# Kernel optimization log

Measured on AMD Instinct MI355X. Metric: run time of the kernel, lower is better.

The kernel has to match this reference:

```python
import jax, jax.numpy as jnp
import numpy as np
from jax import lax

C = 64; H = 128; W = 256; HW = H * W
HIDDEN = 64
D_STATE = 64; HEADDIM = 64; EXPAND = 2; CHUNK = 256; CONV_K = 4
D_INNER = EXPAND * C            # 128
NHEADS = D_INNER // HEADDIM     # 2
CONV_DIM = D_INNER + 2 * D_STATE  # 256
D_IN_PROJ = 2 * D_INNER + 2 * D_STATE + NHEADS  # 386
RECORD_LEN = [5, 3, 4, 2]
EPS = 1e-5


def setup_inputs() -> dict:
    key = jax.random.key(0)
    ks = jax.random.split(key, 16)
    def nrm(k, shape, scale=0.02):
        return scale * jax.random.normal(k, shape, jnp.float32)
    return {
        "xx": jax.random.normal(ks[0], (sum(RECORD_LEN), C, H, W), jnp.float32),
        "record_len": jnp.array(RECORD_LEN, jnp.int32),
        "score_w1": nrm(ks[1], (HIDDEN, C)),
        "score_b1": jnp.zeros((HIDDEN,), jnp.float32),
        "score_w2": nrm(ks[2], (1, HIDDEN)),
        "score_b2": jnp.zeros((1,), jnp.float32),
        "q_w": nrm(ks[3], (C, C)), "q_b": jnp.zeros((C,), jnp.float32),
        "k_w": nrm(ks[4], (C, C)), "k_b": jnp.zeros((C,), jnp.float32),
        "v_w": nrm(ks[5], (C, C)), "v_b": jnp.zeros((C,), jnp.float32),
        "ln_w": jnp.ones((C,), jnp.float32), "ln_b": jnp.zeros((C,), jnp.float32),
        "in_proj_w": nrm(ks[6], (D_IN_PROJ, C)),
        "in_proj_b": jnp.zeros((D_IN_PROJ,), jnp.float32),
        "conv_w": nrm(ks[7], (CONV_DIM, 1, CONV_K), 0.1),
        "conv_b": jnp.zeros((CONV_DIM,), jnp.float32),
        "dt_bias": 0.1 * jax.random.normal(ks[8], (NHEADS,), jnp.float32),
        "A_log": jnp.log(jnp.arange(1, NHEADS + 1, dtype=jnp.float32)),
        "ssd_D": jnp.ones((NHEADS,), jnp.float32),
        "rms_w": jnp.ones((D_INNER,), jnp.float32),
        "out_proj_w": nrm(ks[9], (C, D_INNER)),
    }


def _segsum(x):
    # x: (..., T) -> (..., T, T) with sum_{j<k<=i} x[k] below diagonal, -inf above
    T = x.shape[-1]
    cs = jnp.cumsum(x, -1)
    ss = cs[..., :, None] - cs[..., None, :]
    return jnp.where(jnp.tril(jnp.ones((T, T), bool)), ss, -jnp.inf)


def _ssd(x, A, Bm, Cm):
    # Mamba2 chunked SSD. x:(b,l,h,p) pre-scaled by dt; A:(b,l,h)=dt*A_head; Bm,Cm:(b,l,n) (ngroups=1)
    b, l, h, p = x.shape
    c = l // CHUNK
    x = x.reshape(b, c, CHUNK, h, p)
    A = A.reshape(b, c, CHUNK, h).transpose(0, 3, 1, 2)            # (b,h,c,cl)
    Bm = Bm.reshape(b, c, CHUNK, -1)
    Cm = Cm.reshape(b, c, CHUNK, -1)
    A_cum = jnp.cumsum(A, -1)
    Lmat = jnp.exp(_segsum(A))                                     # (b,h,c,cl,cl)
    Y_diag = jnp.einsum('bcln,bcsn,bhcls,bcshp->bclhp', Cm, Bm, Lmat, x)
    decay_states = jnp.exp(A_cum[..., -1:] - A_cum)                # (b,h,c,cl)
    states = jnp.einsum('bcln,bhcl,bclhp->bchpn', Bm, decay_states, x)
    padded = jnp.pad(A_cum[..., -1], ((0, 0), (0, 0), (1, 0)))     # (b,h,c+1)
    decay_chunk = jnp.exp(_segsum(padded))                         # (b,h,c+1,c+1)
    states_cat = jnp.concatenate([jnp.zeros_like(states[:, :1]), states], 1)
    states_in = jnp.einsum('bhzc,bchpn->bzhpn', decay_chunk, states_cat)[:, :-1]
    Y_off = jnp.einsum('bcln,bchpn,bhcl->bclhp', Cm, states_in, jnp.exp(A_cum))
    return (Y_diag + Y_off).reshape(b, l, h, p)


def _forward(xx, record_len, score_w1, score_b1, score_w2, score_b2,
             q_w, q_b, k_w, k_b, v_w, v_b, ln_w, ln_b,
             in_proj_w, in_proj_b, conv_w, conv_b,
             dt_bias, A_log, ssd_D, rms_w, out_proj_w):
    rl = [int(v) for v in np.asarray(record_len)]
    # score_mlp: 1x1 convs == per-pixel channel MLP, applied to all CAVs at once
    s = jax.nn.relu(jnp.einsum('nchw,dc->ndhw', xx, score_w1) + score_b1[None, :, None, None])
    scores = (jnp.einsum('ndhw,od->nohw', s, score_w2) + score_b2[None, :, None, None])[:, 0]  # (N,H,W)
    fused = []
    start = 0
    for n in rl:  # ragged groups (variable n_cav per sample)
        grp_sc = scores[start:start + n]
        idx = jnp.argmax(grp_sc, axis=0)  # topk k=1; softmax over singleton -> weight 1
        fused.append(jnp.take_along_axis(xx[start:start + n], idx[None, None], axis=0)[0])
        start += n
    fused = jnp.stack(fused)  # (B,C,H,W)
    Bsz = fused.shape[0]
    seq = fused.reshape(Bsz, C, HW).transpose(0, 2, 1)  # (B,L,C)
    # ScaledDotProductAttention on (HW,1,C): each position attends only to itself
    q = seq @ q_w.T + q_b
    k = seq @ k_w.T + k_b
    v = seq @ v_w.T + v_b
    score = jnp.sum(q * k, -1, keepdims=True) / np.float32(np.sqrt(C))  # (B,L,1)
    attn = jax.nn.softmax(score[..., None], axis=-1)[..., 0]            # == 1
    ctx = attn * v
    # VMAMBA2 block: pre-LayerNorm -> Mamba2 SSD -> residual
    mu = jnp.mean(ctx, -1, keepdims=True)
    var = jnp.var(ctx, -1, keepdims=True)
    u = (ctx - mu) / jnp.sqrt(var + EPS) * ln_w + ln_b
    zxbcdt = u @ in_proj_w.T + in_proj_b
    z = zxbcdt[..., :D_INNER]
    xBC = zxbcdt[..., D_INNER:D_INNER + CONV_DIM]
    dt = zxbcdt[..., D_INNER + CONV_DIM:]
    xBC = lax.conv_general_dilated(xBC.transpose(0, 2, 1), conv_w, (1,), [(CONV_K - 1, 0)],
                                   dimension_numbers=('NCH', 'OIH', 'NCH'),
                                   feature_group_count=CONV_DIM)
    xBC = jax.nn.silu(xBC + conv_b[None, :, None]).transpose(0, 2, 1)  # (B,L,CONV_DIM)
    xh = xBC[..., :D_INNER].reshape(Bsz, HW, NHEADS, HEADDIM)
    Bm = xBC[..., D_INNER:D_INNER + D_STATE]
    Cm = xBC[..., D_INNER + D_STATE:]
    dt = jax.nn.softplus(dt + dt_bias)  # (B,L,h)
    A = -jnp.exp(A_log)                 # (h,)
    y = _ssd(xh * dt[..., None], dt * A, Bm, Cm)
    y = y + ssd_D[None, None, :, None] * xh
    y = y.reshape(Bsz, HW, D_INNER)
    yz = y * jax.nn.silu(z)             # gated RMSNorm
    y = yz * lax.rsqrt(jnp.mean(yz * yz, -1, keepdims=True) + EPS) * rms_w
    h = ctx + y @ out_proj_w.T
    return h.transpose(0, 2, 1).reshape(Bsz, C, H, W)


def reference(xx, record_len, score_w1, score_b1, score_w2, score_b2,
              q_w, q_b, k_w, k_b, v_w, v_b, ln_w, ln_b,
              in_proj_w, in_proj_b, conv_w, conv_b,
              dt_bias, A_log, ssd_D, rms_w, out_proj_w):
    return _forward(xx, record_len, score_w1, score_b1, score_w2, score_b2,
                    q_w, q_b, k_w, k_b, v_w, v_b, ln_w, ln_b,
                    in_proj_w, in_proj_b, conv_w, conv_b,
                    dt_bias, A_log, ssd_D, rms_w, out_proj_w)
```

## Files before the change

kernel.cpp:

```cpp
#include <hip/hip_runtime.h>
#include <cmath>

#define HW 32768
#define NC 128
#define NH 2
#define B4 4

typedef __attribute__((ext_vector_type(8))) short bf16x8;
typedef __attribute__((ext_vector_type(4))) float f32x4;
typedef __attribute__((ext_vector_type(4))) ushort u16x4;
typedef __attribute__((ext_vector_type(8))) ushort u16x8;

__device__ __forceinline__ ushort f2b(float x) {
  union { float f; unsigned u; } v; v.f = x;
  unsigned r = v.u + 0x7FFFu + ((v.u >> 16) & 1u);
  return (ushort)(r >> 16);
}
__device__ __forceinline__ float b2f(ushort b) {
  union { unsigned u; float f; } v; v.u = ((unsigned)b) << 16;
  return v.f;
}
__device__ __forceinline__ int swz(int row, int k) { return k ^ ((row & 7) << 3); }
__device__ __forceinline__ bf16x8 ldfrag(const ushort* base, int row, int k, int stride) {
  return *(const bf16x8*)(base + row * stride + swz(row, k));
}

__global__ __launch_bounds__(256) void k_score_mfma(
    const float* __restrict__ xx, const float* __restrict__ w1,
    const float* __restrict__ b1, const float* __restrict__ w2,
    const float* __restrict__ b2, float* __restrict__ scores,
    int* __restrict__ cnt)
{
  __shared__ ushort Whi[64*64];
  __shared__ ushort Wlo[64*64];
  __shared__ ushort Xt[4][64*64];
  __shared__ float w2b1[128];
  int tid = threadIdx.x;
  if (blockIdx.x == 0 && tid == 0) cnt[0] = 0;
  for (int i = tid; i < 4096; i += 256) {
    int d = i >> 6, c = i & 63;
    float v = w1[i];
    ushort hi = f2b(v);
    int off = d*64 + swz(d, c);
    Whi[off] = hi;
    Wlo[off] = f2b(v - b2f(hi));
  }
  if (tid < 64) { w2b1[tid] = w2[tid]; w2b1[64+tid] = b1[tid]; }

  int wid = tid >> 6, lane = tid & 63;
  int n  = blockIdx.x >> 7;
  int t0 = (blockIdx.x & 127)*256 + wid*64;

  {
    const float* px = xx + (size_t)n*64*HW + t0 + lane;
    float xv[64];
    #pragma unroll
    for (int c = 0; c < 64; ++c) xv[c] = px[(size_t)c*HW];
    ushort* xh = Xt[wid];
    #pragma unroll
    for (int c8 = 0; c8 < 8; ++c8) {
      u16x8 p;
      #pragma unroll
      for (int j = 0; j < 8; ++j) p[j] = f2b(xv[c8*8 + j]);
      *(u16x8*)(xh + lane*64 + swz(lane, c8*8)) = p;
    }
  }
  __syncthreads();

  int lr = lane & 15, kb = lane >> 4;
  const ushort* xh = Xt[wid];
  f32x4 acc[4][4];
  #pragma unroll
  for (int m = 0; m < 4; ++m)
    #pragma unroll
    for (int nt = 0; nt < 4; ++nt) acc[m][nt] = (f32x4){0.f,0.f,0.f,0.f};
  #pragma unroll
  for (int k0 = 0; k0 < 64; k0 += 32) {
    bf16x8 ah[4], al[4], bx[4];
    #pragma unroll
    for (int m = 0; m < 4; ++m) {
      ah[m] = ldfrag(Whi, 16*m + lr, k0 + kb*8, 64);
      al[m] = ldfrag(Wlo, 16*m + lr, k0 + kb*8, 64);
    }
    #pragma unroll
    for (int nt = 0; nt < 4; ++nt) bx[nt] = ldfrag(xh, 16*nt + lr, k0 + kb*8, 64);
    #pragma unroll
    for (int m = 0; m < 4; ++m)
      #pragma unroll
      for (int nt = 0; nt < 4; ++nt) {
        acc[m][nt] = __builtin_amdgcn_mfma_f32_16x16x32_bf16(ah[m], bx[nt], acc[m][nt], 0, 0, 0);
        acc[m][nt] = __builtin_amdgcn_mfma_f32_16x16x32_bf16(al[m], bx[nt], acc[m][nt], 0, 0, 0);
      }
  }
  float bb2 = b2[0];
  #pragma unroll
  for (int nt = 0; nt < 4; ++nt) {
    float s = 0.f;
    #pragma unroll
    for (int m = 0; m < 4; ++m)
      #pragma unroll
      for (int r = 0; r < 4; ++r) {
        int d = 16*m + kb*4 + r;
        float h = acc[m][nt][r] + w2b1[64 + d];
        s += fmaxf(h, 0.f) * w2b1[d];
      }
    s += __shfl_xor(s, 16);
    s += __shfl_xor(s, 32);
    if (kb == 0) scores[(size_t)n*HW + t0 + 16*nt + lr] = s + bb2;
  }
}

__global__ __launch_bounds__(256) void k_argmax(
    const float* __restrict__ scores, int* __restrict__ idx,
    int* __restrict__ cnt, int* __restrict__ list)
{
  int i = blockIdx.x*256 + threadIdx.x;
  int g = i >> 15, t = i & (HW-1);
  const int gs0[4] = {0,5,8,12};
  const int gl0[4] = {5,3,4,2};
  int start = gs0[g], len = gl0[g];
  float best = scores[(size_t)start*HW + t];
  float second = -3.4e38f;
  int bi = start;
  for (int j = 1; j < len; ++j) {
    float s = scores[(size_t)(start+j)*HW + t];
    if (s > best) { second = best; best = s; bi = start + j; }
    else if (s > second) second = s;
  }
  idx[i] = bi;
  if (best - second < 5e-4f) {
    int p = atomicAdd(cnt, 1);
    list[p] = i;
  }
}

__global__ __launch_bounds__(256) void k_fix(
    const float* __restrict__ xx, const float* __restrict__ w1,
    const float* __restrict__ b1, const float* __restrict__ w2,
    const float* __restrict__ b2, const int* __restrict__ cnt,
    const int* __restrict__ list, int* __restrict__ idx)
{
  __shared__ float w1f[64*65];
  __shared__ float w2f[64], b1f[64];
  int tid = threadIdx.x;
  for (int i = tid; i < 4096; i += 256) w1f[(i >> 6)*65 + (i & 63)] = w1[i];
  if (tid < 64) { w2f[tid] = w2[tid]; b1f[tid] = b1[tid]; }
  __syncthreads();
  int n = cnt[0];
  int wid = tid >> 6, lane = tid & 63;
  int nwaves = gridDim.x * 4;
  const int gs0[4] = {0,5,8,12};
  const int gl0[4] = {5,3,4,2};
  double b2d = (double)b2[0];
  for (int e = blockIdx.x*4 + wid; e < n; e += nwaves) {
    int i = list[e];
    int g = i >> 15, t = i & (HW-1);
    int start = gs0[g], len = gl0[g];
    double best = -1e300;
    int bi = start;
    for (int j = 0; j < len; ++j) {
      double xv = (double)xx[(size_t)(start+j)*64*HW + (size_t)lane*HW + t];
      double acc = (double)b1f[lane];
      #pragma unroll
      for (int c = 0; c < 64; ++c) {
        double xc = __shfl(xv, c);
        acc += xc * (double)w1f[lane*65 + c];
      }
      double sc = (acc > 0.0 ? acc : 0.0) * (double)w2f[lane];
      #pragma unroll
      for (int m = 1; m < 64; m <<= 1) sc += __shfl_xor(sc, m);
      sc += b2d;
      if (sc > best) { best = sc; bi = start + j; }
    }
    if (lane == 0) idx[i] = bi;
  }
}

__global__ __launch_bounds__(256) void k_fuse(
    const float* __restrict__ xx, const int* __restrict__ idx,
    float* __restrict__ seq)
{
  __shared__ int idxs[64];
  __shared__ float tile[64*65];
  int tid = threadIdx.x;
  int g  = blockIdx.x >> 9;
  int t0 = (blockIdx.x & 511) << 6;
  if (tid < 64) idxs[tid] = idx[(size_t)g*HW + t0 + tid];
  __syncthreads();
  int tl = tid & 63, cq = tid >> 6;
  for (int r = 0; r < 16; ++r) {
    int c = r*4 + cq;
    tile[c*65 + tl] = xx[(size_t)idxs[tl]*64*HW + (size_t)c*HW + t0 + tl];
  }
  __syncthreads();
  for (int r = 0; r < 16; ++r) {
    int row = r*4 + cq;
    seq[((size_t)g*HW + t0 + row)*64 + tl] = tile[tl*65 + row];
  }
}

__global__ __launch_bounds__(256) void k_vln(
    const float* __restrict__ seq, const float* __restrict__ vw,
    const float* __restrict__ vb, const float* __restrict__ lnw,
    const float* __restrict__ lnb, float* __restrict__ ctx,
    ushort* __restrict__ usw)
{
  __shared__ float st[64*64];
  int tid = threadIdx.x;
  size_t p0 = (size_t)blockIdx.x * 64;
  for (int i = tid; i < 64*64; i += 256) st[i] = seq[p0*64 + i];
  int o = tid & 63, wv = tid >> 6;
  float w[64];
  const float4* w4 = (const float4*)(vw + o*64);
  #pragma unroll
  for (int c4 = 0; c4 < 16; ++c4) {
    float4 v = w4[c4];
    w[c4*4+0]=v.x; w[c4*4+1]=v.y; w[c4*4+2]=v.z; w[c4*4+3]=v.w;
  }
  float bias = vb[o], lw = lnw[o], lb = lnb[o];
  __syncthreads();
  const float4* st4 = (const float4*)st;
  for (int j = 0; j < 16; ++j) {
    int p = wv*16 + j;
    float acc = bias;
    #pragma unroll
    for (int c4 = 0; c4 < 16; ++c4) {
      float4 s4 = st4[p*16 + c4];
      acc += s4.x*w[c4*4] + s4.y*w[c4*4+1] + s4.z*w[c4*4+2] + s4.w*w[c4*4+3];
    }
    float s1 = acc, s2 = acc*acc;
    #pragma unroll
    for (int m = 1; m < 64; m <<= 1) {
      s1 += __shfl_xor(s1, m);
      s2 += __shfl_xor(s2, m);
    }
    float mu  = s1*(1.f/64.f);
    float var = s2*(1.f/64.f) - mu*mu;
    float rstd = rsqrtf(var + 1e-5f);
    size_t base = (p0+p)*64;
    int gt = (int)(p0 + p);
    ctx[base + o] = acc;
    usw[base + (o ^ (((gt+3)&7)<<3))] = f2b((acc - mu)*rstd*lw + lb);
  }
}

__global__ __launch_bounds__(256) void k_prep(
    const float* __restrict__ ipw, ushort* __restrict__ wsw)
{
  int i = blockIdx.x*256 + threadIdx.x;
  int row = i >> 6, c = i & 63;
  float v = (row < 386) ? ipw[row*64 + c] : 0.f;
  wsw[row*64 + swz(row, c)] = f2b(v);
}

__global__ __launch_bounds__(512) void k_gemm(
    const ushort* __restrict__ usw, const ushort* __restrict__ wsw,
    const float* __restrict__ ipb, const float* __restrict__ dtbias,
    ushort* __restrict__ z, ushort* __restrict__ xbcB, float* __restrict__ dt)
{
  __shared__ ushort Wlds[400*64];
  __shared__ ushort Ulds[80*64];
  __shared__ ushort trans[8704];
  int tid = threadIdx.x;
  int b  = blockIdx.x >> 9;
  int s  = blockIdx.x & 511;
  int t0 = s << 6;
  size_t pixbase = (size_t)b*HW + t0;
  size_t tilebase = ((size_t)(b*512 + s))*256*64;

  for (int i = tid; i < 3200; i += 512)
    *(u16x8*)(Wlds + i*8) = *(const u16x8*)(wsw + i*8);
  {
    const ushort* ubase = usw + ((size_t)b*HW + t0 - 3)*64;
    for (int i = tid; i < 536; i += 512) {
      u16x8 v;
      if (t0 == 0 && i < 24) v = (u16x8){0,0,0,0,0,0,0,0};
      else v = *(const u16x8*)(ubase + i*8);
      *(u16x8*)(Ulds + i*8) = v;
    }
  }
  __syncthreads();

  int w = tid >> 6, lane = tid & 63, lr = lane & 15, kb = lane >> 4;
  for (int rd = 0; rd < 3; ++rd) {
    int nt = rd*8 + w;
    f32x4 acc[5];
    #pragma unroll
    for (int mt = 0; mt < 5; ++mt) acc[mt] = (f32x4){0.f,0.f,0.f,0.f};
    #pragma unroll
    for (int kk = 0; kk < 64; kk += 32) {
      bf16x8 bfrag = ldfrag(Wlds, nt*16 + lr, kk + kb*8, 64);
      #pragma unroll
      for (int mt = 0; mt < 5; ++mt) {
        bf16x8 afrag = ldfrag(Ulds, mt*16 + lr, kk + kb*8, 64);
        acc[mt] = __builtin_amdgcn_mfma_f32_16x16x32_bf16(afrag, bfrag, acc[mt], 0, 0, 0);
      }
    }
    float bias = ipb[nt*16 + lr];
    if (rd == 0) {
      #pragma unroll
      for (int mt = 0; mt < 5; ++mt)
        #pragma unroll
        for (int r = 0; r < 4; ++r) {
          int t = mt*16 + kb*4 + r - 3;
          if (t >= 0 && t < 64) trans[t*132 + w*16 + lr] = f2b(acc[mt][r] + bias);
        }
    } else {
      #pragma unroll
      for (int mt = 0; mt < 5; ++mt)
        #pragma unroll
        for (int r = 0; r < 4; ++r) {
          int t = mt*16 + kb*4 + r - 3;
          if (t >= 0 && t < 64) trans[(w*16 + lr)*68 + t] = f2b(acc[mt][r] + bias);
        }
    }
    __syncthreads();
    if (rd == 0) {
      for (int i = tid; i < 2048; i += 512) {
        int t = i >> 5, c4 = (i & 31)*4;
        *(u16x4*)(z + (pixbase + t)*128 + c4) = *(const u16x4*)(trans + t*132 + c4);
      }
    } else {
      int chbase = (rd - 1)*128;
      for (int i = tid; i < 2048; i += 512) {
        int ch = i >> 4, t4 = (i & 15)*4;
        *(u16x4*)(xbcB + tilebase + (size_t)(chbase + ch)*64 + t4)
            = *(const u16x4*)(trans + ch*68 + t4);
      }
    }
    __syncthreads();
  }

  if (w == 0) {
    f32x4 acc[5];
    #pragma unroll
    for (int mt = 0; mt < 5; ++mt) acc[mt] = (f32x4){0.f,0.f,0.f,0.f};
    #pragma unroll
    for (int kk = 0; kk < 64; kk += 32) {
      bf16x8 bfrag = ldfrag(Wlds, 384 + lr, kk + kb*8, 64);
      #pragma unroll
      for (int mt = 0; mt < 5; ++mt) {
        bf16x8 afrag = ldfrag(Ulds, mt*16 + lr, kk + kb*8, 64);
        acc[mt] = __builtin_amdgcn_mfma_f32_16x16x32_bf16(afrag, bfrag, acc[mt], 0, 0, 0);
      }
    }
    if (lr < 2) {
      float bias = ipb[384 + lr] + dtbias[lr];
      #pragma unroll
      for (int mt = 0; mt < 5; ++mt)
        #pragma unroll
        for (int r = 0; r < 4; ++r) {
          int t = mt*16 + kb*4 + r - 3;
          if (t >= 0 && t < 64) {
            float a = acc[mt][r] + bias;
            dt[(pixbase + t)*2 + lr] = (a > 20.f) ? a : log1pf(expf(a));
          }
        }
    }
  }
}

__global__ __launch_bounds__(256) void k_conv(
    const ushort* __restrict__ xbcB, const float* __restrict__ convw,
    const float* __restrict__ convb, ushort* __restrict__ co2,
    ushort* __restrict__ Bm, ushort* __restrict__ Cm)
{
  __shared__ ushort bmc[64*132];
  int tid = threadIdx.x;
  int b  = blockIdx.x >> 9;
  int s  = blockIdx.x & 511;
  int lane = tid & 63, wv = tid >> 6;
  int toct = lane & 7, chi = lane >> 3;
  size_t tilebase = ((size_t)(b*512 + s))*256*64;
  const ushort* tsrc = xbcB + tilebase;
  const ushort* psrc = xbcB + tilebase - 256*64;

  for (int it = 0; it < 8; ++it) {
    int ch = wv*64 + it*8 + chi;
    u16x8 v = *(const u16x8*)(tsrc + ch*64 + toct*8);
    float x0 = b2f(v[0]), x1 = b2f(v[1]), x2 = b2f(v[2]), x3 = b2f(v[3]);
    float x4 = b2f(v[4]), x5 = b2f(v[5]), x6 = b2f(v[6]), x7 = b2f(v[7]);
    float pm1 = __shfl(x7, lane - 1);
    float pm2 = __shfl(x6, lane - 1);
    float pm3 = __shfl(x5, lane - 1);
    if (toct == 0) {
      if (s > 0) {
        u16x4 hq = *(const u16x4*)(psrc + ch*64 + 60);
        pm3 = b2f(hq[1]); pm2 = b2f(hq[2]); pm1 = b2f(hq[3]);
      } else {
        pm1 = pm2 = pm3 = 0.f;
      }
    }
    float4 cw = ((const float4*)convw)[ch];
    float cb = convb[ch];
    float o0 = cb + cw.x*pm3 + cw.y*pm2 + cw.z*pm1 + cw.w*x0;
    float o1 = cb + cw.x*pm2 + cw.y*pm1 + cw.z*x0  + cw.w*x1;
    float o2 = cb + cw.x*pm1 + cw.y*x0  + cw.z*x1  + cw.w*x2;
    float o3 = cb + cw.x*x0  + cw.y*x1  + cw.z*x2  + cw.w*x3;
    float o4 = cb + cw.x*x1  + cw.y*x2  + cw.z*x3  + cw.w*x4;
    float o5 = cb + cw.x*x2  + cw.y*x3  + cw.z*x4  + cw.w*x5;
    float o6 = cb + cw.x*x3  + cw.y*x4  + cw.z*x5  + cw.w*x6;
    float o7 = cb + cw.x*x4  + cw.y*x5  + cw.z*x6  + cw.w*x7;
    u16x8 ov;
    ov[0] = f2b(o0 / (1.f + __expf(-o0)));
    ov[1] = f2b(o1 / (1.f + __expf(-o1)));
    ov[2] = f2b(o2 / (1.f + __expf(-o2)));
    ov[3] = f2b(o3 / (1.f + __expf(-o3)));
    ov[4] = f2b(o4 / (1.f + __expf(-o4)));
    ov[5] = f2b(o5 / (1.f + __expf(-o5)));
    ov[6] = f2b(o6 / (1.f + __expf(-o6)));
    ov[7] = f2b(o7 / (1.f + __expf(-o7)));
    *(u16x8*)(co2 + tilebase + (size_t)ch*64 + toct*8) = ov;
    if (ch >= 128) {
      int c = ch - 128;
      int csw = c ^ (toct << 2);
      #pragma unroll
      for (int j = 0; j < 8; ++j)
        bmc[(toct*8 + j)*132 + csw] = ov[j];
    }
  }
  __syncthreads();
  size_t tg = (size_t)b*HW + s*64;
  for (int i = tid; i < 1024; i += 256) {
    int tt = i >> 4, n4 = (i & 15)*4;
    int sw = (tt >> 3) << 2;
    *(u16x4*)(Bm + (tg + tt)*64 + n4) = *(const u16x4*)(bmc + tt*132 + (n4 ^ sw));
    *(u16x4*)(Cm + (tg + tt)*64 + n4) = *(const u16x4*)(bmc + tt*132 + ((64 + n4) ^ sw));
  }
}

__global__ __launch_bounds__(256) void k_states(
    const float* __restrict__ dt, const ushort* __restrict__ co2,
    const float* __restrict__ A_log,
    float* __restrict__ states, float* __restrict__ A_last)
{
  extern __shared__ char smem[];
  float* ac  = (float*)smem;
  float* dec = ac + 256;
  ushort* xdT = (ushort*)(dec + 256);
  ushort* BT  = xdT + 16384;
  int tid = threadIdx.x;
  int ci = blockIdx.x, h = blockIdx.y, b = blockIdx.z;
  size_t tg = (size_t)b*HW + (size_t)ci*256;
  float Aneg = -expf(A_log[h]);
  float dv = dt[(tg + tid)*2 + h];
  ac[tid] = dv*Aneg;
  __syncthreads();
  for (int off = 1; off < 256; off <<= 1) {
    float v = (tid >= off) ? ac[tid - off] : 0.f;
    __syncthreads();
    ac[tid] += v;
    __syncthreads();
  }
  float alast = ac[255];
  dec[tid] = dv * __expf(alast - ac[tid]);
  __syncthreads();
  for (int i = tid; i < 64*32; i += 256) {
    int p = i >> 5, lc = (i & 31) * 8;
    int s = (ci << 2) + (lc >> 6);
    const ushort* cb2 = co2 + ((size_t)(b*512 + s))*256*64 + (lc & 63);
    u16x8 xv = *(const u16x8*)(cb2 + (size_t)(h*64 + p)*64);
    u16x8 o;
    #pragma unroll
    for (int e = 0; e < 8; ++e) o[e] = f2b(b2f(xv[e]) * dec[lc + e]);
    *(u16x8*)(xdT + p*256 + swz(p, lc)) = o;
    u16x8 bv = *(const u16x8*)(cb2 + (size_t)(128 + p)*64);
    *(u16x8*)(BT + p*256 + swz(p, lc)) = bv;
  }
  __syncthreads();
  int w = tid >> 6, lane = tid & 63, lr = lane & 15, kb = lane >> 4;
  f32x4 acc[4];
  #pragma unroll
  for (int m = 0; m < 4; ++m) acc[m] = (f32x4){0.f,0.f,0.f,0.f};
  for (int k0 = 0; k0 < 256; k0 += 32) {
    bf16x8 bfrag = ldfrag(BT, 16*w + lr, k0 + kb*8, 256);
    #pragma unroll
    for (int m = 0; m < 4; ++m) {
      bf16x8 afrag = ldfrag(xdT, 16*m + lr, k0 + kb*8, 256);
      acc[m] = __builtin_amdgcn_mfma_f32_16x16x32_bf16(afrag, bfrag, acc[m], 0, 0, 0);
    }
  }
  size_t sb = (((size_t)b*NC + ci)*NH + h)*4096;
  #pragma unroll
  for (int m = 0; m < 4; ++m)
    #pragma unroll
    for (int r = 0; r < 4; ++r)
      states[sb + (size_t)(16*m + kb*4 + r)*64 + 16*w + lr] = acc[m][r];
  if (tid == 0) A_last[((size_t)b*NH + h)*NC + ci] = alast;
}

__global__ __launch_bounds__(256) void k_scan(
    const float* __restrict__ states, const float* __restrict__ A_last,
    float* __restrict__ states_in)
{
  __shared__ float ef[NC];
  int tid = threadIdx.x;
  int seg = blockIdx.x & 7, h = (blockIdx.x >> 3) & 1, b = blockIdx.x >> 4;
  if (tid < NC) ef[tid] = __expf(A_last[((size_t)b*NH + h)*NC + tid]);
  __syncthreads();
  size_t base0 = (((size_t)b*NC)*NH + h)*4096 + seg*512 + tid;
  const size_t cstride = (size_t)NH*4096;
  float s0 = 0.f, s1 = 0.f;
  float ld0 = states[base0], ld1 = states[base0 + 256];
  for (int zc = 0; zc < NC; ++zc) {
    size_t cur = base0 + (size_t)zc*cstride;
    float n0 = 0.f, n1 = 0.f;
    if (zc < NC-1) { n0 = states[cur + cstride]; n1 = states[cur + cstride + 256]; }
    states_in[cur] = s0; states_in[cur + 256] = s1;
    float e = ef[zc];
    s0 = ld0 + e*s0; s1 = ld1 + e*s1;
    ld0 = n0; ld1 = n1;
  }
}

__global__ __launch_bounds__(512) void k_ydiag(
    const float* __restrict__ dt, const ushort* __restrict__ co2,
    const ushort* __restrict__ Bm, const ushort* __restrict__ Cm,
    const float* __restrict__ states_in, const float* __restrict__ A_log,
    const float* __restrict__ ssd_D, ushort* __restrict__ y)
{
  extern __shared__ char smem[];
  float* ac   = (float*)smem;
  float* dts  = ac + 256;
  float* segs = dts + 256;
  ushort* Cb  = (ushort*)(segs + 8);
  ushort* Bb  = Cb + 16384;
  ushort* xsT = Bb + 16384;
  ushort* Sb  = xsT + 16384;
  ushort* Wb  = Sb + 4096;
  int tid = threadIdx.x;
  int ci = blockIdx.x, h = blockIdx.y, b = blockIdx.z;
  size_t tg = (size_t)b*HW + (size_t)ci*256;
  int w = tid >> 6, lane = tid & 63, lr = lane & 15, kb = lane >> 4;
  float Aneg = -expf(A_log[h]);

  float dv = 0.f, a = 0.f;
  if (tid < 256) {
    dv = dt[(tg + tid)*2 + h];
    a = dv*Aneg;
    #pragma unroll
    for (int d = 1; d < 64; d <<= 1) {
      float t = __shfl_up(a, d);
      if (lane >= d) a += t;
    }
    if (lane == 63) segs[w] = a;
  }
  __syncthreads();
  if (tid < 256) {
    float off = 0.f;
    #pragma unroll
    for (int j = 0; j < 4; ++j) if (j < w) off += segs[j];
    ac[tid] = a + off;
    dts[tid] = dv;
  }
  __syncthreads();

  for (int i = tid; i < 256*16; i += 512) {
    int l = i >> 4, n4 = (i & 15) * 4;
    u16x4 cv = *(const u16x4*)(Cm + (tg + l)*64 + n4);
    *(u16x4*)(Cb + l*64 + swz(l, n4)) = cv;
    u16x4 bv = *(const u16x4*)(Bm + (tg + l)*64 + n4);
    *(u16x4*)(Bb + l*64 + swz(l, n4)) = bv;
  }
  for (int i = tid; i < 64*32; i += 512) {
    int p = i >> 5, sc = (i & 31) * 8;
    int s = (ci << 2) + (sc >> 6);
    u16x8 xv = *(const u16x8*)(co2 + ((size_t)(b*512 + s)*256 + h*64 + p)*64 + (sc & 63));
    u16x8 o;
    #pragma unroll
    for (int e = 0; e < 8; ++e) o[e] = f2b(b2f(xv[e]) * dts[sc + e]);
    *(u16x8*)(xsT + p*256 + swz(p, sc)) = o;
  }
  size_t sbg = (((size_t)b*NC + ci)*NH + h)*4096;
  for (int i = tid; i < 1024; i += 512) {
    int p = i >> 4, n4 = (i & 15) * 4;
    float4 sv = *(const float4*)(states_in + sbg + p*64 + n4);
    u16x4 pk = { f2b(sv.x), f2b(sv.y), f2b(sv.z), f2b(sv.w) };
    *(u16x4*)(Sb + p*64 + swz(p, n4)) = pk;
  }
  __syncthreads();

  int l0 = w*32;
  ushort* Ww = Wb + w*2048;

  f32x4 yy[2][4];
  #pragma unroll
  for (int m = 0; m < 2; ++m)
    #pragma unroll
    for (int n = 0; n < 4; ++n) yy[m][n] = (f32x4){0.f,0.f,0.f,0.f};
  #pragma unroll
  for (int kk = 0; kk < 64; kk += 32) {
    bf16x8 af[2], bf[4];
    #pragma unroll
    for (int m = 0; m < 2; ++m) af[m] = ldfrag(Cb, l0 + 16*m + lr, kk + kb*8, 64);
    #pragma unroll
    for (int n = 0; n < 4; ++n) bf[n] = ldfrag(Sb, 16*n + lr, kk + kb*8, 64);
    #pragma unroll
    for (int m = 0; m < 2; ++m)
      #pragma unroll
      for (int n = 0; n < 4; ++n)
        yy[m][n] = __builtin_amdgcn_mfma_f32_16x16x32_bf16(af[m], bf[n], yy[m][n], 0, 0, 0);
  }
  #pragma unroll
  for (int m = 0; m < 2; ++m)
    #pragma unroll
    for (int r = 0; r < 4; ++r) {
      float e = __expf(ac[l0 + 16*m + kb*4 + r]);
      #pragma unroll
      for (int n = 0; n < 4; ++n) yy[m][n][r] *= e;
    }

  int nst = (w >> 1) + 1;
  for (int st = 0; st < nst; ++st) {
    int s0 = st*64;
    f32x4 g[2][4];
    #pragma unroll
    for (int m = 0; m < 2; ++m)
      #pragma unroll
      for (int n = 0; n < 4; ++n) g[m][n] = (f32x4){0.f,0.f,0.f,0.f};
    #pragma unroll
    for (int kk = 0; kk < 64; kk += 32) {
      bf16x8 af[2], bf[4];
      #pragma unroll
      for (int m = 0; m < 2; ++m) af[m] = ldfrag(Cb, l0 + 16*m + lr, kk + kb*8, 64);
      #pragma unroll
      for (int n = 0; n < 4; ++n) bf[n] = ldfrag(Bb, s0 + 16*n + lr, kk + kb*8, 64);
      #pragma unroll
      for (int m = 0; m < 2; ++m)
        #pragma unroll
        for (int n = 0; n < 4; ++n)
          g[m][n] = __builtin_amdgcn_mfma_f32_16x16x32_bf16(af[m], bf[n], g[m][n], 0, 0, 0);
    }
    #pragma unroll
    for (int m = 0; m < 2; ++m)
      #pragma unroll
      for (int r = 0; r < 4; ++r) {
        int lrow = 16*m + kb*4 + r;
        int lg = l0 + lrow;
        float acl = ac[lg];
        #pragma unroll
        for (int n = 0; n < 4; ++n) {
          int sl = 16*n + lr;
          int sg = s0 + sl;
          float v = (sg <= lg) ? g[m][n][r] * __expf(acl - ac[sg]) : 0.f;
          Ww[lrow*64 + swz(lrow, sl)] = f2b(v);
        }
      }
    #pragma unroll
    for (int kk = 0; kk < 64; kk += 32) {
      bf16x8 af[2], bf[4];
      #pragma unroll
      for (int m = 0; m < 2; ++m) af[m] = ldfrag(Ww, 16*m + lr, kk + kb*8, 64);
      #pragma unroll
      for (int n = 0; n < 4; ++n) bf[n] = ldfrag(xsT, 16*n + lr, s0 + kk + kb*8, 256);
      #pragma unroll
      for (int m = 0; m < 2; ++m)
        #pragma unroll
        for (int n = 0; n < 4; ++n)
          yy[m][n] = __builtin_amdgcn_mfma_f32_16x16x32_bf16(af[m], bf[n], yy[m][n], 0, 0, 0);
    }
  }

  float Dh = ssd_D[h];
  #pragma unroll
  for (int m = 0; m < 2; ++m)
    #pragma unroll
    for (int r = 0; r < 4; ++r) {
      int lg = l0 + 16*m + kb*4 + r;
      float f = Dh / dts[lg];
      #pragma unroll
      for (int n = 0; n < 4; ++n) {
        int p = 16*n + lr;
        float val = yy[m][n][r] + f * b2f(xsT[p*256 + swz(p, lg)]);
        y[(tg + lg)*128 + h*64 + p] = f2b(val);
      }
    }
}

__global__ __launch_bounds__(256) void k_final(
    const ushort* __restrict__ y, const ushort* __restrict__ z,
    const float* __restrict__ ctx, const float* __restrict__ rms_w,
    const float* __restrict__ opw, float* __restrict__ out)
{
  __shared__ ushort yn[64*128];
  __shared__ ushort wop[64*128];
  __shared__ float otile[64*65];
  int tid = threadIdx.x;
  size_t p0 = (size_t)blockIdx.x * 64;

  for (int i = tid; i < 2048; i += 256) {
    int row = i >> 5, c4 = (i & 31) * 4;
    float4 v = ((const float4*)(opw + row*128))[c4 >> 2];
    float4 rw = ((const float4*)rms_w)[c4 >> 2];
    u16x4 p = { f2b(v.x*rw.x), f2b(v.y*rw.y), f2b(v.z*rw.z), f2b(v.w*rw.w) };
    *(u16x4*)(wop + row*128 + swz(row, c4)) = p;
  }

  {
    int t = tid >> 2, q = tid & 3;
    const u16x4* yp = (const u16x4*)(y + (p0 + t)*128 + q*32);
    const u16x4* zp = (const u16x4*)(z + (p0 + t)*128 + q*32);
    float vals[32];
    float ss = 0.f;
    #pragma unroll
    for (int j = 0; j < 8; ++j) {
      u16x4 yv = yp[j];
      u16x4 zv = zp[j];
      #pragma unroll
      for (int e = 0; e < 4; ++e) {
        float zf = b2f(zv[e]);
        float x = b2f(yv[e]) * (zf / (1.f + __expf(-zf)));
        vals[j*4+e] = x; ss += x*x;
      }
    }
    ss += __shfl_xor(ss, 1);
    ss += __shfl_xor(ss, 2);
    float rinv = rsqrtf(ss*(1.f/128.f) + 1e-5f);
    #pragma unroll
    for (int j = 0; j < 8; ++j) {
      int c4 = q*32 + j*4;
      u16x4 p = { f2b(vals[j*4]*rinv), f2b(vals[j*4+1]*rinv),
                  f2b(vals[j*4+2]*rinv), f2b(vals[j*4+3]*rinv) };
      *(u16x4*)(yn + t*128 + swz(t, c4)) = p;
    }
  }
  __syncthreads();

  int w = tid >> 6, lane = tid & 63, lr = lane & 15, kb = lane >> 4;
  f32x4 acc[4];
  #pragma unroll
  for (int n = 0; n < 4; ++n) acc[n] = (f32x4){0.f,0.f,0.f,0.f};
  #pragma unroll
  for (int kk = 0; kk < 128; kk += 32) {
    bf16x8 a = ldfrag(yn, w*16 + lr, kk + kb*8, 128);
    #pragma unroll
    for (int n = 0; n < 4; ++n) {
      bf16x8 bf = ldfrag(wop, n*16 + lr, kk + kb*8, 128);
      acc[n] = __builtin_amdgcn_mfma_f32_16x16x32_bf16(a, bf, acc[n], 0, 0, 0);
    }
  }
  #pragma unroll
  for (int n = 0; n < 4; ++n)
    #pragma unroll
    for (int r = 0; r < 4; ++r) {
      int tok = w*16 + kb*4 + r, ch = n*16 + lr;
      otile[ch*65 + tok] = acc[n][r] + ctx[(p0 + tok)*64 + ch];
    }
  __syncthreads();
  {
    size_t b  = p0 >> 15;
    size_t t0 = p0 & (HW-1);
    for (int r = 0; r < 16; ++r) {
      int cc = r*4 + (tid >> 6);
      int pp = tid & 63;
      out[(b*64 + cc)*HW + t0 + pp] = otile[cc*65 + pp];
    }
  }
}

extern "C" void kernel_launch(void* const* d_in, const int* in_sizes, int n_in,
                              void* d_out, int out_size, void* d_ws, size_t ws_size,
                              hipStream_t stream) {
  (void)in_sizes; (void)n_in; (void)out_size; (void)ws_size;
  const float* xx   = (const float*)d_in[0];
  const float* sw1  = (const float*)d_in[2];
  const float* sb1  = (const float*)d_in[3];
  const float* sw2  = (const float*)d_in[4];
  const float* sb2  = (const float*)d_in[5];
  const float* vw   = (const float*)d_in[10];
  const float* vb   = (const float*)d_in[11];
  const float* lnw  = (const float*)d_in[12];
  const float* lnb  = (const float*)d_in[13];
  const float* ipw  = (const float*)d_in[14];
  const float* ipb  = (const float*)d_in[15];
  const float* cw   = (const float*)d_in[16];
  const float* cb   = (const float*)d_in[17];
  const float* dtb  = (const float*)d_in[18];
  const float* alog = (const float*)d_in[19];
  const float* sd   = (const float*)d_in[20];
  const float* rmsw = (const float*)d_in[21];
  const float* opw  = (const float*)d_in[22];

  float* ws = (float*)d_ws;
  float*  scores32 = ws;
  int*    idxb     = (int*)(ws + 458752);
  int*    cntb     = (int*)(ws + 589824);
  int*    listb    = (int*)(ws + 589832);
  float*  dtp      = ws;
  float*  seq      = ws + 917504;
  ushort* Cmb      = (ushort*)(ws + 917504);
  ushort* Bmb      = (ushort*)(ws + 5111808);
  float*  ctx      = ws + 9306112;
  ushort* uswb     = (ushort*)(ws + 17694720);
  float*  states   = ws + 17694720;
  float*  states_in= ws + 21889024;
  ushort* zb       = (ushort*)(ws + 26083328);
  ushort* xbcBb    = (ushort*)(ws + 34471936);
  ushort* co2b     = (ushort*)(ws + 51249152);
  ushort* yb       = (ushort*)(ws + 68026368);
  float*  Alast    = ws + 84803584;
  ushort* wswb     = (ushort*)(ws + 84804608);

  k_score_mfma<<<1792, 256, 0, stream>>>(xx, sw1, sb1, sw2, sb2, scores32, cntb);
  k_argmax<<<512, 256, 0, stream>>>(scores32, idxb, cntb, listb);
  k_fix<<<512, 256, 0, stream>>>(xx, sw1, sb1, sw2, sb2, cntb, listb, idxb);
  k_fuse<<<2048, 256, 0, stream>>>(xx, idxb, seq);
  k_vln<<<2048, 256, 0, stream>>>(seq, vw, vb, lnw, lnb, ctx, uswb);
  k_prep<<<100, 256, 0, stream>>>(ipw, wswb);
  k_gemm<<<2048, 512, 0, stream>>>(uswb, wswb, ipb, dtb, zb, xbcBb, dtp);
  k_conv<<<2048, 256, 0, stream>>>(xbcBb, cw, cb, co2b, Bmb, Cmb);
  dim3 gssd(NC, NH, B4);
  k_states<<<gssd, 256, 67584, stream>>>(dtp, co2b, alog, states, Alast);
  k_scan<<<64, 256, 0, stream>>>(states, Alast, states_in);
  k_ydiag<<<gssd, 512, 141344, stream>>>(dtp, co2b, Bmb, Cmb, states_in, alog, sd, yb);
  k_final<<<2048, 256, 0, stream>>>(yb, zb, ctx, rmsw, opw, (float*)d_out);
}
```

Baseline: 419.1 us.

## Shrink k_ydiag shared memory by reading B, x and states from global

Stops staging B, the dt-scaled x tile and the chunk states in LDS inside k_ydiag. MFMA fragments are now loaded straight from global memory: states are converted to bf16 on the fly, B and x (co2) are read unscaled, and the dt scaling moves into the W matrix so D*x needs no division. The padded W layout replaces the swizzle. LDS per block roughly halves, which should let more blocks share a CU and removes one barrier and the staging loops. In exchange, fragment loads become uncoalesced global/L2 reads that repeat across waves, and the rounding point of x*dt changes slightly.

```diff
diff --git a/kernel.cpp b/kernel.cpp
--- a/kernel.cpp
+++ b/kernel.cpp
@@ -524,10 +524,7 @@
   float* dts  = ac + 256;
   float* segs = dts + 256;
   ushort* Cb  = (ushort*)(segs + 8);
-  ushort* Bb  = Cb + 16384;
-  ushort* xsT = Bb + 16384;
-  ushort* Sb  = xsT + 16384;
-  ushort* Wb  = Sb + 4096;
+  ushort* Wb  = Cb + 16384;
   int tid = threadIdx.x;
   int ci = blockIdx.x, h = blockIdx.y, b = blockIdx.z;
   size_t tg = (size_t)b*HW + (size_t)ci*256;
@@ -553,35 +550,17 @@
     ac[tid] = a + off;
     dts[tid] = dv;
   }
-  __syncthreads();
-
   for (int i = tid; i < 256*16; i += 512) {
     int l = i >> 4, n4 = (i & 15) * 4;
     u16x4 cv = *(const u16x4*)(Cm + (tg + l)*64 + n4);
     *(u16x4*)(Cb + l*64 + swz(l, n4)) = cv;
-    u16x4 bv = *(const u16x4*)(Bm + (tg + l)*64 + n4);
-    *(u16x4*)(Bb + l*64 + swz(l, n4)) = bv;
-  }
-  for (int i = tid; i < 64*32; i += 512) {
-    int p = i >> 5, sc = (i & 31) * 8;
-    int s = (ci << 2) + (sc >> 6);
-    u16x8 xv = *(const u16x8*)(co2 + ((size_t)(b*512 + s)*256 + h*64 + p)*64 + (sc & 63));
-    u16x8 o;
-    #pragma unroll
-    for (int e = 0; e < 8; ++e) o[e] = f2b(b2f(xv[e]) * dts[sc + e]);
-    *(u16x8*)(xsT + p*256 + swz(p, sc)) = o;
-  }
+  }
+  __syncthreads();
+
+  int l0 = w*32;
+  ushort* Ww = Wb + w*2304;
   size_t sbg = (((size_t)b*NC + ci)*NH + h)*4096;
-  for (int i = tid; i < 1024; i += 512) {
-    int p = i >> 4, n4 = (i & 15) * 4;
-    float4 sv = *(const float4*)(states_in + sbg + p*64 + n4);
-    u16x4 pk = { f2b(sv.x), f2b(sv.y), f2b(sv.z), f2b(sv.w) };
-    *(u16x4*)(Sb + p*64 + swz(p, n4)) = pk;
-  }
-  __syncthreads();
-
-  int l0 = w*32;
-  ushort* Ww = Wb + w*2048;
+  const ushort* ct0 = co2 + ((size_t)(b*512 + (ci << 2)))*16384 + (size_t)h*4096;
 
   f32x4 yy[2][4];
   #pragma unroll
@@ -594,7 +573,14 @@
     #pragma unroll
     for (int m = 0; m < 2; ++m) af[m] = ldfrag(Cb, l0 + 16*m + lr, kk + kb*8, 64);
     #pragma unroll
-    for (int n = 0; n < 4; ++n) bf[n] = ldfrag(Sb, 16*n + lr, kk + kb*8, 64);
+    for (int n = 0; n < 4; ++n) {
+      const float4* sp = (const float4*)(states_in + sbg + (size_t)(16*n + lr)*64 + kk + kb*8);
+      float4 s1 = sp[0], s2 = sp[1];
+      u16x8 pk;
+      pk[0]=f2b(s1.x); pk[1]=f2b(s1.y); pk[2]=f2b(s1.z); pk[3]=f2b(s1.w);
+      pk[4]=f2b(s2.x); pk[5]=f2b(s2.y); pk[6]=f2b(s2.z); pk[7]=f2b(s2.w);
+      bf[n] = *(bf16x8*)&pk;
+    }
     #pragma unroll
     for (int m = 0; m < 2; ++m)
       #pragma unroll
@@ -624,7 +610,8 @@
       #pragma unroll
       for (int m = 0; m < 2; ++m) af[m] = ldfrag(Cb, l0 + 16*m + lr, kk + kb*8, 64);
       #pragma unroll
-      for (int n = 0; n < 4; ++n) bf[n] = ldfrag(Bb, s0 + 16*n + lr, kk + kb*8, 64);
+      for (int n = 0; n < 4; ++n)
+        bf[n] = *(const bf16x8*)(Bm + (tg + s0 + 16*n + lr)*64 + kk + kb*8);
       #pragma unroll
       for (int m = 0; m < 2; ++m)
         #pragma unroll
@@ -642,17 +629,20 @@
         for (int n = 0; n < 4; ++n) {
           int sl = 16*n + lr;
           int sg = s0 + sl;
-          float v = (sg <= lg) ? g[m][n][r] * __expf(acl - ac[sg]) : 0.f;
-          Ww[lrow*64 + swz(lrow, sl)] = f2b(v);
+          float v = (sg <= lg) ? g[m][n][r] * __expf(acl - ac[sg]) * dts[sg] : 0.f;
+          Ww[lrow*72 + sl] = f2b(v);
         }
       }
+    const ushort* xt = ct0 + (size_t)st*16384;
     #pragma unroll
     for (int kk = 0; kk < 64; kk += 32) {
       bf16x8 af[2], bf[4];
       #pragma unroll
-      for (int m = 0; m < 2; ++m) af[m] = ldfrag(Ww, 16*m + lr, kk + kb*8, 64);
-      #pragma unroll
-      for (int n = 0; n < 4; ++n) bf[n] = ldfrag(xsT, 16*n + lr, s0 + kk + kb*8, 256);
+      for (int m = 0; m < 2; ++m)
+        af[m] = *(const bf16x8*)(Ww + (16*m + lr)*72 + kk + kb*8);
+      #pragma unroll
+      for (int n = 0; n < 4; ++n)
+        bf[n] = *(const bf16x8*)(xt + (size_t)(16*n + lr)*64 + kk + kb*8);
       #pragma unroll
       for (int m = 0; m < 2; ++m)
         #pragma unroll
@@ -667,11 +657,12 @@
     #pragma unroll
     for (int r = 0; r < 4; ++r) {
       int lg = l0 + 16*m + kb*4 + r;
-      float f = Dh / dts[lg];
+      const ushort* xlt = ct0 + (size_t)(lg >> 6)*16384;
+      int lc = lg & 63;
       #pragma unroll
       for (int n = 0; n < 4; ++n) {
         int p = 16*n + lr;
-        float val = yy[m][n][r] + f * b2f(xsT[p*256 + swz(p, lg)]);
+        float val = yy[m][n][r] + Dh * b2f(xlt[(size_t)p*64 + lc]);
         y[(tg + lg)*128 + h*64 + p] = f2b(val);
       }
     }
@@ -812,6 +803,6 @@
   dim3 gssd(NC, NH, B4);
   k_states<<<gssd, 256, 67584, stream>>>(dtp, co2b, alog, states, Alast);
   k_scan<<<64, 256, 0, stream>>>(states, Alast, states_in);
-  k_ydiag<<<gssd, 512, 141344, stream>>>(dtp, co2b, Bmb, Cmb, states_in, alog, sd, yb);
+  k_ydiag<<<gssd, 512, 71712, stream>>>(dtp, co2b, Bmb, Cmb, states_in, alog, sd, yb);
   k_final<<<2048, 256, 0, stream>>>(yb, zb, ctx, rmsw, opw, (float*)d_out);
 }
```

Result: slower. 451.8 us (+7.8%).
